# Optimization experiments

Measured on AMD Instinct MI355X. Metric: run time of the kernel, lower is better.

## Reference

```python
import jax, jax.numpy as jnp
import numpy as np

BS, N, H, W = 32, 8, 512, 512

def setup_inputs() -> dict:
    key = jax.random.key(0)
    k1, k2, k3 = jax.random.split(key, 3)
    pred_iou = jax.random.uniform(k1, (BS, N), dtype=jnp.float32)
    target_masks = jax.random.randint(k2, (BS, H, W), 0, 2, dtype=jnp.int32)
    pred_masks = jax.random.uniform(k3, (BS, N, H, W), dtype=jnp.float32)
    return {"pred_iou": pred_iou, "target_masks": target_masks, "pred_masks": pred_masks}

def reference(pred_iou, target_masks, pred_masks):
    # Binary Jaccard (torchmetrics): threshold preds at 0.5, target > 0.
    pred_bin = pred_masks > 0.5                      # [bs, n, H, W]
    tgt_bin = (target_masks > 0)[:, None, :, :]      # [bs, 1, H, W] broadcast over n
    inter = jnp.sum(pred_bin & tgt_bin, axis=(-2, -1)).astype(jnp.float32)  # [bs, n]
    union = jnp.sum(pred_bin | tgt_bin, axis=(-2, -1)).astype(jnp.float32)  # [bs, n]
    actual_iou = jnp.where(union > 0, inter / jnp.maximum(union, 1.0), 0.0)  # [bs, n]
    squared_error = (pred_iou - actual_iou) ** 2
    return squared_error
```

## Files before the change

kernel.cpp:

```cpp
#include <hip/hip_runtime.h>


#define BS      32
#define NMASKS  8
#define HW      (512 * 512)
#define CHUNKS  64
#define BLOCK   256
#define NPAIRS  (BS * NMASKS)
#define CHUNK_ELEMS (HW / CHUNKS)
#define VEC_ITERS   (CHUNK_ELEMS / (BLOCK * 4))

typedef int   iv4 __attribute__((ext_vector_type(4)));
typedef float fv4 __attribute__((ext_vector_type(4)));

__global__ __launch_bounds__(BLOCK) void iou_count_kernel(
    const int* __restrict__ tgt,
    const float* __restrict__ pred,
    unsigned long long* __restrict__ ws)
{
    const int b     = blockIdx.x >> 6;
    const int chunk = blockIdx.x & (CHUNKS - 1);
    const int tid   = threadIdx.x;

    const size_t tgt_base  = (size_t)b * HW + (size_t)chunk * CHUNK_ELEMS;
    const size_t pred_base = (size_t)b * NMASKS * HW + (size_t)chunk * CHUNK_ELEMS;

    unsigned int inter[NMASKS];
    unsigned int uni[NMASKS];
#pragma unroll
    for (int n = 0; n < NMASKS; ++n) { inter[n] = 0u; uni[n] = 0u; }

#pragma unroll
    for (int it = 0; it < VEC_ITERS; ++it) {
        const size_t off = (size_t)it * (BLOCK * 4) + (size_t)tid * 4;

        const iv4 t4 = __builtin_nontemporal_load((const iv4*)(tgt + tgt_base + off));
        const int tb0 = t4.x > 0, tb1 = t4.y > 0, tb2 = t4.z > 0, tb3 = t4.w > 0;

        fv4 p[NMASKS];
#pragma unroll
        for (int n = 0; n < NMASKS; ++n)
            p[n] = __builtin_nontemporal_load(
                (const fv4*)(pred + pred_base + (size_t)n * HW + off));

#pragma unroll
        for (int n = 0; n < NMASKS; ++n) {
            const int pb0 = p[n].x > 0.5f;
            const int pb1 = p[n].y > 0.5f;
            const int pb2 = p[n].z > 0.5f;
            const int pb3 = p[n].w > 0.5f;
            inter[n] += (unsigned)((pb0 & tb0) + (pb1 & tb1) + (pb2 & tb2) + (pb3 & tb3));
            uni[n]   += (unsigned)((pb0 | tb0) + (pb1 | tb1) + (pb2 | tb2) + (pb3 | tb3));
        }
    }

    const int lane = tid & 63;
    const int wave = tid >> 6;
    __shared__ unsigned long long s[BLOCK / 64][NMASKS];

#pragma unroll
    for (int n = 0; n < NMASKS; ++n) {
        unsigned long long v =
            ((unsigned long long)inter[n] << 32) | (unsigned long long)uni[n];
#pragma unroll
        for (int off = 32; off > 0; off >>= 1)
            v += __shfl_down(v, off);
        if (lane == 0) s[wave][n] = v;
    }
    __syncthreads();

    if (tid < NMASKS) {
        unsigned long long v = s[0][tid] + s[1][tid] + s[2][tid] + s[3][tid];
        ws[(size_t)chunk * NPAIRS + (size_t)b * NMASKS + tid] = v;
    }
}

__global__ __launch_bounds__(NPAIRS) void finalize_kernel(
    const float* __restrict__ pred_iou,
    const unsigned long long* __restrict__ ws,
    float* __restrict__ out)
{
    const int i = threadIdx.x;
    unsigned long long v = 0ull;
#pragma unroll
    for (int c = 0; c < CHUNKS; ++c)
        v += ws[(size_t)c * NPAIRS + i];

    const unsigned int inter = (unsigned int)(v >> 32);
    const unsigned int uni   = (unsigned int)(v & 0xffffffffu);
    const float iou = (uni > 0u) ? ((float)inter / (float)uni) : 0.0f;
    const float d = pred_iou[i] - iou;
    out[i] = d * d;
}

extern "C" void kernel_launch(void* const* d_in, const int* in_sizes, int n_in,
                              void* d_out, int out_size, void* d_ws, size_t ws_size,
                              hipStream_t stream) {
    const float* pred_iou = (const float*)d_in[0];
    const int*   tgt      = (const int*)d_in[1];
    const float* pred     = (const float*)d_in[2];
    float* out = (float*)d_out;
    unsigned long long* ws = (unsigned long long*)d_ws;

    iou_count_kernel<<<BS * CHUNKS, BLOCK, 0, stream>>>(tgt, pred, ws);
    finalize_kernel<<<1, NPAIRS, 0, stream>>>(pred_iou, ws, out);
}
```

Baseline: 358.6 us.

## Assign one mask per block and split spatial range into groups

Restructures the count kernel so each block processes a single (batch, mask) pair over one eighth of the image, instead of all eight masks over a small chunk. This cuts per-thread register usage, since one accumulator pair replaces eight, and the launch bounds are raised to allow more resident blocks. In exchange, the target mask is read eight times, once per mask, relying on cache reuse. The finalize kernel now sums 8 partial groups instead of 64.

```diff
diff --git a/kernel.cpp b/kernel.cpp
--- a/kernel.cpp
+++ b/kernel.cpp
@@ -4,75 +4,63 @@
 #define BS      32
 #define NMASKS  8
 #define HW      (512 * 512)
-#define CHUNKS  64
+#define GROUPS  8
+#define SPAN    (HW / GROUPS)
 #define BLOCK   256
 #define NPAIRS  (BS * NMASKS)
-#define CHUNK_ELEMS (HW / CHUNKS)
-#define VEC_ITERS   (CHUNK_ELEMS / (BLOCK * 4))
+#define PER_THREAD (SPAN / (BLOCK * 4))
 
 typedef int   iv4 __attribute__((ext_vector_type(4)));
 typedef float fv4 __attribute__((ext_vector_type(4)));
 
-__global__ __launch_bounds__(BLOCK) void iou_count_kernel(
+__global__ __launch_bounds__(BLOCK, 8) void iou_count_kernel(
     const int* __restrict__ tgt,
     const float* __restrict__ pred,
     unsigned long long* __restrict__ ws)
 {
-    const int b     = blockIdx.x >> 6;
-    const int chunk = blockIdx.x & (CHUNKS - 1);
-    const int tid   = threadIdx.x;
+    const int idx = blockIdx.x;
+    const int b   = idx >> 6;
+    const int n   = (idx >> 3) & 7;
+    const int grp = idx & 7;
+    const int tid = threadIdx.x;
 
-    const size_t tgt_base  = (size_t)b * HW + (size_t)chunk * CHUNK_ELEMS;
-    const size_t pred_base = (size_t)b * NMASKS * HW + (size_t)chunk * CHUNK_ELEMS;
+    const size_t tgt_base  = (size_t)b * HW + (size_t)grp * SPAN;
+    const size_t pred_base = ((size_t)b * NMASKS + n) * HW + (size_t)grp * SPAN;
 
-    unsigned int inter[NMASKS];
-    unsigned int uni[NMASKS];
-#pragma unroll
-    for (int n = 0; n < NMASKS; ++n) { inter[n] = 0u; uni[n] = 0u; }
+    unsigned int inter = 0u, uni = 0u;
 
-#pragma unroll
-    for (int it = 0; it < VEC_ITERS; ++it) {
+#pragma unroll 4
+    for (int it = 0; it < PER_THREAD; ++it) {
         const size_t off = (size_t)it * (BLOCK * 4) + (size_t)tid * 4;
 
-        const iv4 t4 = __builtin_nontemporal_load((const iv4*)(tgt + tgt_base + off));
+        const iv4 t4 = *(const iv4*)(tgt + tgt_base + off);
+        const fv4 p4 = __builtin_nontemporal_load(
+            (const fv4*)(pred + pred_base + off));
+
         const int tb0 = t4.x > 0, tb1 = t4.y > 0, tb2 = t4.z > 0, tb3 = t4.w > 0;
+        const int pb0 = p4.x > 0.5f, pb1 = p4.y > 0.5f,
+                  pb2 = p4.z > 0.5f, pb3 = p4.w > 0.5f;
 
-        fv4 p[NMASKS];
-#pragma unroll
-        for (int n = 0; n < NMASKS; ++n)
-            p[n] = __builtin_nontemporal_load(
-                (const fv4*)(pred + pred_base + (size_t)n * HW + off));
+        inter += (unsigned)((pb0 & tb0) + (pb1 & tb1) + (pb2 & tb2) + (pb3 & tb3));
+        uni   += (unsigned)((pb0 | tb0) + (pb1 | tb1) + (pb2 | tb2) + (pb3 | tb3));
+    }
 
-#pragma unroll
-        for (int n = 0; n < NMASKS; ++n) {
-            const int pb0 = p[n].x > 0.5f;
-            const int pb1 = p[n].y > 0.5f;
-            const int pb2 = p[n].z > 0.5f;
-            const int pb3 = p[n].w > 0.5f;
-            inter[n] += (unsigned)((pb0 & tb0) + (pb1 & tb1) + (pb2 & tb2) + (pb3 & tb3));
-            uni[n]   += (unsigned)((pb0 | tb0) + (pb1 | tb1) + (pb2 | tb2) + (pb3 | tb3));
-        }
-    }
+    unsigned long long v =
+        ((unsigned long long)inter << 32) | (unsigned long long)uni;
 
     const int lane = tid & 63;
     const int wave = tid >> 6;
-    __shared__ unsigned long long s[BLOCK / 64][NMASKS];
+    __shared__ unsigned long long s[BLOCK / 64];
 
 #pragma unroll
-    for (int n = 0; n < NMASKS; ++n) {
-        unsigned long long v =
-            ((unsigned long long)inter[n] << 32) | (unsigned long long)uni[n];
-#pragma unroll
-        for (int off = 32; off > 0; off >>= 1)
-            v += __shfl_down(v, off);
-        if (lane == 0) s[wave][n] = v;
-    }
+    for (int off = 32; off > 0; off >>= 1)
+        v += __shfl_down(v, off);
+    if (lane == 0) s[wave] = v;
     __syncthreads();
 
-    if (tid < NMASKS) {
-        unsigned long long v = s[0][tid] + s[1][tid] + s[2][tid] + s[3][tid];
-        ws[(size_t)chunk * NPAIRS + (size_t)b * NMASKS + tid] = v;
-    }
+    if (tid == 0)
+        ws[(size_t)grp * NPAIRS + (size_t)b * NMASKS + n] =
+            s[0] + s[1] + s[2] + s[3];
 }
 
 __global__ __launch_bounds__(NPAIRS) void finalize_kernel(
@@ -83,8 +71,8 @@
     const int i = threadIdx.x;
     unsigned long long v = 0ull;
 #pragma unroll
-    for (int c = 0; c < CHUNKS; ++c)
-        v += ws[(size_t)c * NPAIRS + i];
+    for (int g = 0; g < GROUPS; ++g)
+        v += ws[(size_t)g * NPAIRS + i];
 
     const unsigned int inter = (unsigned int)(v >> 32);
     const unsigned int uni   = (unsigned int)(v & 0xffffffffu);
@@ -102,6 +90,6 @@
     float* out = (float*)d_out;
     unsigned long long* ws = (unsigned long long*)d_ws;
 
-    iou_count_kernel<<<BS * CHUNKS, BLOCK, 0, stream>>>(tgt, pred, ws);
+    iou_count_kernel<<<BS * NMASKS * GROUPS, BLOCK, 0, stream>>>(tgt, pred, ws);
     finalize_kernel<<<1, NPAIRS, 0, stream>>>(pred_iou, ws, out);
 }
```

Result: slower. 368.7 us (+2.8%).
